# Performance work log

Hardware: AMD Instinct MI355X
Metric: run time of the kernel (lower is better)

## Reference

```python
import jax, jax.numpy as jnp
import numpy as np


def setup_inputs() -> dict:
    key = jax.random.key(0)
    k1, k2 = jax.random.split(key)
    queries = jax.random.normal(k1, (16, 1024, 256), dtype=jnp.float32)
    embedding = jax.random.normal(k2, (8192, 256), dtype=jnp.float32) * 0.02
    return {"queries": queries, "embedding": embedding}


def reference(queries, embedding):
    commitment_weight = 0.25
    # squared L2 distances: ||q||^2 + ||e||^2 - 2 q.e  -> [b, k, n]
    q_sq = jnp.sum(queries * queries, axis=-1, keepdims=True)          # [b,k,1]
    e_sq = jnp.sum(embedding * embedding, axis=-1)[None, None, :]      # [1,1,n]
    distances = q_sq + e_sq - 2.0 * jnp.einsum('bkc,nc->bkn', queries, embedding)
    code_indices = jnp.argmin(distances, axis=-1)                      # [b,k] int
    quantized = embedding[code_indices]                                # [b,k,c]
    commit_loss = jnp.mean((jax.lax.stop_gradient(queries) - quantized) ** 2)
    codebook_loss = jnp.mean((queries - jax.lax.stop_gradient(quantized)) ** 2)
    vq_loss = codebook_loss + commitment_weight * commit_loss
    # straight-through estimator
    quantized_st = queries + jax.lax.stop_gradient(quantized - queries)
    return (code_indices, quantized_st, vq_loss)
```

## Files before the change

### kernel.cpp

```cpp
#include <hip/hip_runtime.h>
#include <float.h>

typedef _Float16 half8 __attribute__((ext_vector_type(8)));
typedef _Float16 half4v __attribute__((ext_vector_type(4)));
typedef float f32x4 __attribute__((ext_vector_type(4)));

#define M_TOTAL 16384
#define N_CODES 8192
#define KDIM    256
#define BM 128
#define BN 256
#define BK 32
#define NK (KDIM / BK)
#define NB (N_CODES / BN)
#define TS 32
#define MARGIN 3.6e-3f
#define SQ_SCALE 512.0f
#define SE_SCALE 2048.0f
#define INV_PROD 1.9073486328125e-06f
#define RG 4
#define RCODES 1024
#define RNCH (N_CODES / RCODES)
#define RPB 1024
#define RM_BLOCKS 256
#define LR_BLOCKS 32

#define PREP_Q_BLOCKS (M_TOTAL / 4)
#define PREP_E_BLOCKS (N_CODES / 4)
#define TR_BLOCKS ((N_CODES / 64) * (KDIM / 64))

__device__ __forceinline__ void prep_body(const float* __restrict__ src,
                                          _Float16* __restrict__ dst,
                                          float* __restrict__ sq, float scale,
                                          int row0, int tid) {
    {
        const int r = row0 + (tid >> 6);
        const int e4 = tid & 63;
        const float4 v = *(const float4*)(src + (size_t)r * KDIM + e4 * 4);
        const half4v h = {(_Float16)(v.x * scale), (_Float16)(v.y * scale),
                          (_Float16)(v.z * scale), (_Float16)(v.w * scale)};
        ((half4v*)(dst + (size_t)r * KDIM))[e4] = h;
    }
    if (tid < 64) {
        const int grp = tid >> 4;
        const int sub = tid & 15;
        const int row = row0 + grp;
        const float* p = src + (size_t)row * KDIM + (sub >> 3) * 128 + (sub & 7);
        float r;
        {
            #pragma clang fp contract(off)
            float v = p[0];
            r = v * v;
            #pragma unroll
            for (int k = 1; k < 16; k++) { const float w = p[k * 8]; r = r + w * w; }
        }
        const float t1 = r  + __shfl_xor(r,  1, 64);
        const float t2 = t1 + __shfl_xor(t1, 2, 64);
        const float t3 = t2 + __shfl_xor(t2, 4, 64);
        const float t4 = t3 + __shfl_xor(t3, 8, 64);
        if (sub == 0) sq[row] = t4;
    }
}

__global__ void prep_fused_kernel(const float* __restrict__ Q, const float* __restrict__ E,
                                  _Float16* __restrict__ Qh, _Float16* __restrict__ Eh,
                                  float* __restrict__ qsq, float* __restrict__ esq,
                                  float* __restrict__ ET) {
    __shared__ float tile[64][65];
    const int tid = threadIdx.x;
    const int b = blockIdx.x;
    if (b < PREP_Q_BLOCKS) {
        prep_body(Q, Qh, qsq, SQ_SCALE, b * 4, tid);
        return;
    }
    if (b < PREP_Q_BLOCKS + PREP_E_BLOCKS) {
        prep_body(E, Eh, esq, SE_SCALE, (b - PREP_Q_BLOCKS) * 4, tid);
        return;
    }
    const int idx = b - PREP_Q_BLOCKS - PREP_E_BLOCKS;
    const int n0 = (idx & 127) * 64;
    const int k0 = (idx >> 7) * 64;
    const int r = tid >> 4;
    const int c4 = tid & 15;
    #pragma unroll
    for (int p = 0; p < 4; p++) {
        const int row = p * 16 + r;
        const float4 v = *(const float4*)(E + (size_t)(n0 + row) * KDIM + k0 + c4 * 4);
        tile[row][c4 * 4 + 0] = v.x;
        tile[row][c4 * 4 + 1] = v.y;
        tile[row][c4 * 4 + 2] = v.z;
        tile[row][c4 * 4 + 3] = v.w;
    }
    __syncthreads();
    #pragma unroll
    for (int p = 0; p < 4; p++) {
        const int d = p * 16 + r;
        float4 o;
        o.x = tile[c4 * 4 + 0][d];
        o.y = tile[c4 * 4 + 1][d];
        o.z = tile[c4 * 4 + 2][d];
        o.w = tile[c4 * 4 + 3][d];
        *(float4*)(ET + (size_t)(k0 + d) * N_CODES + n0 + c4 * 4) = o;
    }
}

union SMemU {
    struct { _Float16 q[3][BM * TS]; _Float16 e[3][BN * TS]; } t;
    struct { unsigned k1[BM][2]; unsigned k2[BM][2]; } red;
};

__device__ __forceinline__ void gl_lds16(const void* g, void* lds) {
    __builtin_amdgcn_global_load_lds(
        (const __attribute__((address_space(1))) unsigned*)g,
        (__attribute__((address_space(3))) unsigned*)lds, 16, 0, 0);
}

__global__ __launch_bounds__(256, 2)
void mfma_top2_kernel(const _Float16* __restrict__ Qh, const _Float16* __restrict__ Eh,
                      const float* __restrict__ esq,
                      unsigned* __restrict__ k1s, unsigned* __restrict__ k2s) {
    __shared__ SMemU sm;
    const int tid = threadIdx.x;
    const int m0 = blockIdx.x * BM;
    const int n0 = blockIdx.y * BN;
    const int w = tid >> 6, lane = tid & 63;
    const int wm = w >> 1, wn = w & 1;
    const int qd = lane >> 4, c = lane & 15;

    const int lrow = lane >> 2;
    const int gsw = (lane & 3) ^ ((lane >> 3) & 3);
    const _Float16* qsrc = Qh + (size_t)(m0 + w * 32 + lrow) * KDIM + gsw * 8;
    const _Float16* esrc = Eh + (size_t)(n0 + w * 64 + lrow) * KDIM + gsw * 8;

    f32x4 acc[4][8];
    const f32x4 zero = {0.f, 0.f, 0.f, 0.f};
    #pragma unroll
    for (int mt = 0; mt < 4; mt++)
        #pragma unroll
        for (int nt = 0; nt < 8; nt++) acc[mt][nt] = zero;

    #define STAGE(buf, kofs) do {                                                  \
        _Float16* qdst = sm.t.q[buf] + w * 1024;                                   \
        _Float16* edst = sm.t.e[buf] + w * 2048;                                   \
        gl_lds16(qsrc + (kofs),             qdst);                                 \
        gl_lds16(qsrc + 16 * KDIM + (kofs), qdst + 512);                           \
        gl_lds16(esrc + (kofs),             edst);                                 \
        gl_lds16(esrc + 16 * KDIM + (kofs), edst + 512);                           \
        gl_lds16(esrc + 32 * KDIM + (kofs), edst + 1024);                          \
        gl_lds16(esrc + 48 * KDIM + (kofs), edst + 1536);                          \
    } while (0)

    STAGE(0, 0);
    STAGE(1, BK);
    STAGE(2, 2 * BK);
    asm volatile("s_waitcnt vmcnt(12)" ::: "memory");
    __builtin_amdgcn_s_barrier();

    const int csw = (c >> 1) & 3;

    #pragma unroll
    for (int ki = 0; ki < NK; ki++) {
        const int buf = ki % 3;
        const _Float16* bq = sm.t.q[buf];
        const _Float16* be = sm.t.e[buf];
        half8 qa[4];
        #pragma unroll
        for (int mt = 0; mt < 4; mt++)
            qa[mt] = *(const half8*)(bq + (wm * 64 + mt * 16 + c) * TS + (qd ^ csw) * 8);
        __builtin_amdgcn_s_setprio(1);
        #pragma unroll
        for (int nt = 0; nt < 8; nt++) {
            const half8 eh = *(const half8*)(be + (wn * 128 + nt * 16 + c) * TS + (qd ^ csw) * 8);
            #pragma unroll
            for (int mt = 0; mt < 4; mt++)
                acc[mt][nt] = __builtin_amdgcn_mfma_f32_16x16x32_f16(qa[mt], eh, acc[mt][nt], 0, 0, 0);
        }
        __builtin_amdgcn_s_setprio(0);
        if (ki == NK - 1) break;
        if (ki <= NK - 3) { asm volatile("s_waitcnt vmcnt(6)" ::: "memory"); }
        else              { asm volatile("s_waitcnt vmcnt(0)" ::: "memory"); }
        __builtin_amdgcn_s_barrier();
        if (ki + 3 < NK) STAGE(buf, (ki + 3) * BK);
    }
    #undef STAGE

    float es8[8];
    #pragma unroll
    for (int nt = 0; nt < 8; nt++) es8[nt] = esq[n0 + wn * 128 + nt * 16 + c] + 8.0f;

    unsigned k1[16], k2[16];
    #pragma unroll
    for (int i = 0; i < 16; i++) { k1[i] = 0xFFFFFFFFu; k2[i] = 0xFFFFFFFFu; }

    #pragma unroll
    for (int mt = 0; mt < 4; mt++)
        #pragma unroll
        for (int nt = 0; nt < 8; nt++) {
            const unsigned nl = (unsigned)(wn * 128 + nt * 16 + c);
            #pragma unroll
            for (int r = 0; r < 4; r++) {
                const int i = mt * 4 + r;
                const float d = fmaf(acc[mt][nt][r], -INV_PROD, es8[nt]);
                const unsigned k = (__float_as_uint(d) & 0xFFFFFF00u) | nl;
                const unsigned t = min(k1[i], k);
                k2[i] = min(k2[i], max(k1[i], k));
                k1[i] = t;
            }
        }
    #pragma unroll
    for (int s = 1; s < 16; s <<= 1) {
        #pragma unroll
        for (int i = 0; i < 16; i++) {
            const unsigned ok1 = (unsigned)__shfl_xor((int)k1[i], s, 64);
            const unsigned ok2 = (unsigned)__shfl_xor((int)k2[i], s, 64);
            const unsigned t = min(k1[i], ok1);
            k2[i] = min(min(k2[i], ok2), max(k1[i], ok1));
            k1[i] = t;
        }
    }
    __syncthreads();
    if (c == 0) {
        #pragma unroll
        for (int mt = 0; mt < 4; mt++)
            #pragma unroll
            for (int r = 0; r < 4; r++) {
                const int ml = wm * 64 + mt * 16 + qd * 4 + r;
                sm.red.k1[ml][wn] = k1[mt * 4 + r];
                sm.red.k2[ml][wn] = k2[mt * 4 + r];
            }
    }
    __syncthreads();
    if (tid < BM) {
        const unsigned a1 = sm.red.k1[tid][0], b1 = sm.red.k1[tid][1];
        const unsigned a2 = sm.red.k2[tid][0], b2 = sm.red.k2[tid][1];
        const size_t o = (size_t)(m0 + tid) * NB + blockIdx.y;
        k1s[o] = min(a1, b1);
        k2s[o] = min(min(a2, b2), max(a1, b1));
    }
}

__global__ void finalize_kernel(const float* __restrict__ Q, const float* __restrict__ E,
                                const unsigned* __restrict__ k1s, const unsigned* __restrict__ k2s,
                                int* __restrict__ fcount, int* __restrict__ flist,
                                float* __restrict__ ws_loss, float* __restrict__ out) {
    const int q = blockIdx.x * 4 + (threadIdx.x >> 6);
    const int lane = threadIdx.x & 63;
    unsigned d1 = 0xFFFFFF00u;
    unsigned d2 = 0xFFFFFF00u;
    int gi = 0x7FFFFFFF;
    if (lane < NB) {
        const unsigned k1 = k1s[(size_t)q * NB + lane];
        const unsigned k2 = k2s[(size_t)q * NB + lane];
        d1 = k1 & 0xFFFFFF00u;
        gi = lane * BN + (int)(k1 & 255u);
        d2 = k2 & 0xFFFFFF00u;
    }
    #pragma unroll
    for (int s = 1; s < 64; s <<= 1) {
        const unsigned od1 = (unsigned)__shfl_xor((int)d1, s, 64);
        const int      ogi = __shfl_xor(gi, s, 64);
        const unsigned od2 = (unsigned)__shfl_xor((int)d2, s, 64);
        const unsigned nd2 = min(min(d2, od2), max(d1, od1));
        const bool take = (od1 < d1) || (od1 == d1 && ogi < gi);
        d1 = take ? od1 : d1;
        gi = take ? ogi : gi;
        d2 = nd2;
    }
    if ((__uint_as_float(d2) - __uint_as_float(d1)) < MARGIN) {
        if (lane == 0) flist[atomicAdd(fcount, 1)] = q;
        return;
    }

    if (lane == 0) out[q] = (float)gi;
    const float4 qv = *(const float4*)(Q + (size_t)q * KDIM + lane * 4);
    const float4 ev = *(const float4*)(E + (size_t)gi * KDIM + lane * 4);
    float4 st;
    {
        #pragma clang fp contract(off)
        st.x = qv.x + (ev.x - qv.x);
        st.y = qv.y + (ev.y - qv.y);
        st.z = qv.z + (ev.z - qv.z);
        st.w = qv.w + (ev.w - qv.w);
    }
    *(float4*)(out + M_TOTAL + (size_t)q * KDIM + lane * 4) = st;

    const float dx = qv.x - ev.x, dy = qv.y - ev.y, dz = qv.z - ev.z, dw = qv.w - ev.w;
    float s = dx * dx + dy * dy + dz * dz + dw * dw;
    #pragma unroll
    for (int off = 32; off > 0; off >>= 1) s += __shfl_down(s, off);
    if (lane == 0) ws_loss[q] = s;
}

__global__ __launch_bounds__(256, 4)
void refine_partial_kernel(const float* __restrict__ Q, const float* __restrict__ ET,
                           const float* __restrict__ qsq, const float* __restrict__ esq,
                           const int* __restrict__ fcount, const int* __restrict__ flist,
                           float* __restrict__ rp_v, int* __restrict__ rp_i) {
    const int cnt = *fcount;
    if (cnt == 0) return;
    const int ngroups = (cnt + RG - 1) / RG;
    const int ntasks = ngroups * RNCH;
    const int tid = threadIdx.x;
    const int w = tid >> 6, lane = tid & 63;
    __shared__ float qs[RG][KDIM];
    __shared__ float redv[4][RG];
    __shared__ int   redi[4][RG];

    for (int t = blockIdx.x; t < ntasks; t += RPB) {
        const int grp = t >> 3;
        const int chunk = t & (RNCH - 1);
        __syncthreads();
        {
            const int g = tid >> 6, c4 = tid & 63;
            const int fi = min(grp * RG + g, cnt - 1);
            const int q = flist[fi];
            *(float4*)&qs[g][c4 * 4] = *(const float4*)(Q + (size_t)q * KDIM + c4 * 4);
        }
        __syncthreads();

        const int nb = chunk * RCODES + tid * 4;
        float a[RG][4];
        #pragma unroll
        for (int g = 0; g < RG; g++)
            #pragma unroll
            for (int j = 0; j < 4; j++) a[g][j] = 0.f;

        for (int k4 = 0; k4 < KDIM / 4; k4++) {
            float4 qv[RG];
            #pragma unroll
            for (int g = 0; g < RG; g++) qv[g] = *(const float4*)&qs[g][k4 * 4];
            #pragma unroll
            for (int kk = 0; kk < 4; kk++) {
                const float4 ev = *(const float4*)(ET + (size_t)(k4 * 4 + kk) * N_CODES + nb);
                #pragma unroll
                for (int g = 0; g < RG; g++) {
                    const float qk = (kk == 0) ? qv[g].x : (kk == 1) ? qv[g].y
                                   : (kk == 2) ? qv[g].z : qv[g].w;
                    a[g][0] = fmaf(qk, ev.x, a[g][0]);
                    a[g][1] = fmaf(qk, ev.y, a[g][1]);
                    a[g][2] = fmaf(qk, ev.z, a[g][2]);
                    a[g][3] = fmaf(qk, ev.w, a[g][3]);
                }
            }
        }

        float es[4];
        #pragma unroll
        for (int j = 0; j < 4; j++) es[j] = esq[nb + j];

        #pragma unroll
        for (int g = 0; g < RG; g++) {
            const int fi = min(grp * RG + g, cnt - 1);
            const float qsv = qsq[flist[fi]];
            float bv = FLT_MAX; int bi = 0x7fffffff;
            #pragma unroll
            for (int j = 0; j < 4; j++) {
                float d;
                {
                    #pragma clang fp contract(off)
                    const float t1 = qsv + es[j];
                    d = t1 - 2.0f * a[g][j];
                }
                if (d < bv) { bv = d; bi = nb + j; }
            }
            #pragma unroll
            for (int s = 1; s < 64; s <<= 1) {
                const float ov = __shfl_xor(bv, s, 64);
                const int   oi = __shfl_xor(bi, s, 64);
                if (ov < bv || (ov == bv && oi < bi)) { bv = ov; bi = oi; }
            }
            if (lane == 0) { redv[w][g] = bv; redi[w][g] = bi; }
        }
        __syncthreads();
        if (tid < RG) {
            float fv = redv[0][tid]; int fidx = redi[0][tid];
            #pragma unroll
            for (int u = 1; u < 4; u++) {
                if (redv[u][tid] < fv || (redv[u][tid] == fv && redi[u][tid] < fidx)) {
                    fv = redv[u][tid]; fidx = redi[u][tid];
                }
            }
            rp_v[(size_t)t * RG + tid] = fv;
            rp_i[(size_t)t * RG + tid] = fidx;
        }
    }
}

__global__ void refine_merge_kernel(const float* __restrict__ Q, const float* __restrict__ E,
                                    const int* __restrict__ fcount, const int* __restrict__ flist,
                                    const float* __restrict__ rp_v, const int* __restrict__ rp_i,
                                    float* __restrict__ ws_loss, float* __restrict__ out) {
    const int cnt = *fcount;
    const int lane = threadIdx.x;
    for (int fi = blockIdx.x; fi < cnt; fi += RM_BLOCKS) {
        const int q = flist[fi];
        const int grp = fi >> 2, g = fi & 3;
        float bv = FLT_MAX; int bi = 0x7fffffff;
        if (lane < RNCH) {
            const size_t t = (size_t)(grp * RNCH + lane);
            bv = rp_v[t * RG + g];
            bi = rp_i[t * RG + g];
        }
        #pragma unroll
        for (int s = 1; s < 64; s <<= 1) {
            const float ov = __shfl_xor(bv, s, 64);
            const int   oi = __shfl_xor(bi, s, 64);
            if (ov < bv || (ov == bv && oi < bi)) { bv = ov; bi = oi; }
        }
        if (lane == 0) out[q] = (float)bi;

        const float4 qv = *(const float4*)(Q + (size_t)q * KDIM + lane * 4);
        const float4 ev = *(const float4*)(E + (size_t)bi * KDIM + lane * 4);
        float4 st;
        {
            #pragma clang fp contract(off)
            st.x = qv.x + (ev.x - qv.x);
            st.y = qv.y + (ev.y - qv.y);
            st.z = qv.z + (ev.z - qv.z);
            st.w = qv.w + (ev.w - qv.w);
        }
        *(float4*)(out + M_TOTAL + (size_t)q * KDIM + lane * 4) = st;
        const float dx = qv.x - ev.x, dy = qv.y - ev.y, dz = qv.z - ev.z, dw = qv.w - ev.w;
        float s = dx * dx + dy * dy + dz * dz + dw * dw;
        #pragma unroll
        for (int off = 32; off > 0; off >>= 1) s += __shfl_down(s, off);
        if (lane == 0) ws_loss[q] = s;
    }
}

__global__ void loss_reduce_kernel(const float* __restrict__ ws_loss, float* __restrict__ out) {
    const int tid = threadIdx.x;
    float s = 0.f;
    for (int i = blockIdx.x * 256 + tid; i < M_TOTAL; i += LR_BLOCKS * 256)
        s += ws_loss[i];
    #pragma unroll
    for (int off = 32; off > 0; off >>= 1) s += __shfl_down(s, off);
    __shared__ float ws[4];
    if ((tid & 63) == 0) ws[tid >> 6] = s;
    __syncthreads();
    if (tid == 0) {
        const float tot = (ws[0] + ws[1]) + (ws[2] + ws[3]);
        atomicAdd(out + M_TOTAL + (size_t)M_TOTAL * KDIM,
                  tot * (1.25f / (float)((size_t)M_TOTAL * KDIM)));
    }
}

extern "C" void kernel_launch(void* const* d_in, const int* in_sizes, int n_in,
                              void* d_out, int out_size, void* d_ws, size_t ws_size,
                              hipStream_t stream) {
    const float* Q = (const float*)d_in[0];
    const float* E = (const float*)d_in[1];
    float* out = (float*)d_out;

    char* ws = (char*)d_ws;
    _Float16* Qh  = (_Float16*)(ws);
    _Float16* Eh  = (_Float16*)(ws + (size_t)8  * 1024 * 1024);
    float* qsq    = (float*)   (ws + (size_t)12 * 1024 * 1024);
    float* esq    = qsq + M_TOTAL;
    unsigned* k1s = (unsigned*)(ws + (size_t)13 * 1024 * 1024);
    unsigned* k2s = (unsigned*)(ws + (size_t)17 * 1024 * 1024);
    int*   fcount = (int*)     (ws + (size_t)25 * 1024 * 1024);
    int*   flist  = fcount + 64;
    float* ws_loss= (float*)   (ws + (size_t)25 * 1024 * 1024 + 512 * 1024);
    float* ET     = (float*)   (ws + (size_t)26 * 1024 * 1024);
    float* rp_v   = (float*)k1s;
    int*   rp_i   = (int*)k2s;

    hipMemsetAsync(out + M_TOTAL + (size_t)M_TOTAL * KDIM, 0, sizeof(float), stream);
    hipMemsetAsync(fcount, 0, sizeof(int), stream);

    prep_fused_kernel<<<PREP_Q_BLOCKS + PREP_E_BLOCKS + TR_BLOCKS, 256, 0, stream>>>(
        Q, E, Qh, Eh, qsq, esq, ET);

    mfma_top2_kernel<<<dim3(M_TOTAL / BM, N_CODES / BN), 256, 0, stream>>>(
        Qh, Eh, esq, k1s, k2s);

    finalize_kernel<<<M_TOTAL / 4, 256, 0, stream>>>(Q, E, k1s, k2s, fcount, flist, ws_loss, out);
    refine_partial_kernel<<<RPB, 256, 0, stream>>>(Q, ET, qsq, esq, fcount, flist, rp_v, rp_i);
    refine_merge_kernel<<<RM_BLOCKS, 64, 0, stream>>>(Q, E, fcount, flist, rp_v, rp_i, ws_loss, out);
    loss_reduce_kernel<<<LR_BLOCKS, 256, 0, stream>>>(ws_loss, out);
}
```

Baseline: 216.9 us.

## Refine only candidate code blocks per flagged query and fuse refine stages

The fp32 refinement of ambiguous queries now scans only the 256-code blocks whose per-block best fp16 distance lies within a margin of the global best, using per-block minima from the top-2 pass, instead of all 8192 codes. The partial and merge refine kernels are fused into one kernel with one block per flagged query, which removes a launch and the intermediate buffers. The two memsets are folded into the prep kernel to cut launch overhead. Correctness now depends on the per-block keys bounding the true minimum within MARGIN. Each query is processed alone, so ET rows are no longer shared across four queries.

```diff
diff --git a/kernel.cpp b/kernel.cpp
--- a/kernel.cpp
+++ b/kernel.cpp
@@ -18,11 +18,7 @@
 #define SQ_SCALE 512.0f
 #define SE_SCALE 2048.0f
 #define INV_PROD 1.9073486328125e-06f
-#define RG 4
-#define RCODES 1024
-#define RNCH (N_CODES / RCODES)
-#define RPB 1024
-#define RM_BLOCKS 256
+#define RB 1024
 #define LR_BLOCKS 32
 
 #define PREP_Q_BLOCKS (M_TOTAL / 4)
@@ -65,10 +61,12 @@
 __global__ void prep_fused_kernel(const float* __restrict__ Q, const float* __restrict__ E,
                                   _Float16* __restrict__ Qh, _Float16* __restrict__ Eh,
                                   float* __restrict__ qsq, float* __restrict__ esq,
-                                  float* __restrict__ ET) {
+                                  float* __restrict__ ET,
+                                  int* __restrict__ fcount, float* __restrict__ loss_slot) {
     __shared__ float tile[64][65];
     const int tid = threadIdx.x;
     const int b = blockIdx.x;
+    if (b == 0 && tid == 0) { *fcount = 0; *loss_slot = 0.f; }
     if (b < PREP_Q_BLOCKS) {
         prep_body(Q, Qh, qsq, SQ_SCALE, b * 4, tid);
         return;
@@ -292,114 +290,57 @@
 }
 
 __global__ __launch_bounds__(256, 4)
-void refine_partial_kernel(const float* __restrict__ Q, const float* __restrict__ ET,
-                           const float* __restrict__ qsq, const float* __restrict__ esq,
-                           const int* __restrict__ fcount, const int* __restrict__ flist,
-                           float* __restrict__ rp_v, int* __restrict__ rp_i) {
+void refine_kernel(const float* __restrict__ Q, const float* __restrict__ E,
+                   const float* __restrict__ ET,
+                   const float* __restrict__ qsq, const float* __restrict__ esq,
+                   const int* __restrict__ fcount, const int* __restrict__ flist,
+                   const unsigned* __restrict__ k1s,
+                   float* __restrict__ ws_loss, float* __restrict__ out) {
     const int cnt = *fcount;
-    if (cnt == 0) return;
-    const int ngroups = (cnt + RG - 1) / RG;
-    const int ntasks = ngroups * RNCH;
     const int tid = threadIdx.x;
     const int w = tid >> 6, lane = tid & 63;
-    __shared__ float qs[RG][KDIM];
-    __shared__ float redv[4][RG];
-    __shared__ int   redi[4][RG];
-
-    for (int t = blockIdx.x; t < ntasks; t += RPB) {
-        const int grp = t >> 3;
-        const int chunk = t & (RNCH - 1);
+    __shared__ float qs[KDIM];
+    __shared__ unsigned cmask_sh;
+    __shared__ float redv[4];
+    __shared__ int   redi[4];
+
+    for (int fi = blockIdx.x; fi < cnt; fi += RB) {
+        const int q = flist[fi];
         __syncthreads();
-        {
-            const int g = tid >> 6, c4 = tid & 63;
-            const int fi = min(grp * RG + g, cnt - 1);
-            const int q = flist[fi];
-            *(float4*)&qs[g][c4 * 4] = *(const float4*)(Q + (size_t)q * KDIM + c4 * 4);
+        qs[tid] = Q[(size_t)q * KDIM + tid];
+        if (w == 0) {
+            unsigned k1 = 0xFFFFFF00u;
+            if (lane < NB) k1 = k1s[(size_t)q * NB + lane];
+            unsigned m = k1;
+            #pragma unroll
+            for (int s = 1; s < 64; s <<= 1)
+                m = min(m, (unsigned)__shfl_xor((int)m, s, 64));
+            const float thr = __uint_as_float(m & 0xFFFFFF00u) + MARGIN;
+            const bool cand = (lane < NB) &&
+                              (__uint_as_float(k1 & 0xFFFFFF00u) < thr);
+            const unsigned long long bal = __ballot(cand);
+            if (lane == 0) cmask_sh = (unsigned)bal;
         }
         __syncthreads();
-
-        const int nb = chunk * RCODES + tid * 4;
-        float a[RG][4];
-        #pragma unroll
-        for (int g = 0; g < RG; g++)
-            #pragma unroll
-            for (int j = 0; j < 4; j++) a[g][j] = 0.f;
-
-        for (int k4 = 0; k4 < KDIM / 4; k4++) {
-            float4 qv[RG];
-            #pragma unroll
-            for (int g = 0; g < RG; g++) qv[g] = *(const float4*)&qs[g][k4 * 4];
-            #pragma unroll
-            for (int kk = 0; kk < 4; kk++) {
-                const float4 ev = *(const float4*)(ET + (size_t)(k4 * 4 + kk) * N_CODES + nb);
-                #pragma unroll
-                for (int g = 0; g < RG; g++) {
-                    const float qk = (kk == 0) ? qv[g].x : (kk == 1) ? qv[g].y
-                                   : (kk == 2) ? qv[g].z : qv[g].w;
-                    a[g][0] = fmaf(qk, ev.x, a[g][0]);
-                    a[g][1] = fmaf(qk, ev.y, a[g][1]);
-                    a[g][2] = fmaf(qk, ev.z, a[g][2]);
-                    a[g][3] = fmaf(qk, ev.w, a[g][3]);
-                }
+        unsigned cmask = cmask_sh;
+        const float qsv = qsq[q];
+        float bv = FLT_MAX;
+        int   bi = 0x7fffffff;
+        while (cmask) {
+            const int cb = __builtin_ctz(cmask);
+            cmask &= cmask - 1;
+            const int n = cb * BN + tid;
+            float a = 0.f;
+            #pragma unroll 8
+            for (int k = 0; k < KDIM; k++)
+                a = fmaf(qs[k], ET[(size_t)k * N_CODES + n], a);
+            float d;
+            {
+                #pragma clang fp contract(off)
+                const float t1 = qsv + esq[n];
+                d = t1 - 2.0f * a;
             }
-        }
-
-        float es[4];
-        #pragma unroll
-        for (int j = 0; j < 4; j++) es[j] = esq[nb + j];
-
-        #pragma unroll
-        for (int g = 0; g < RG; g++) {
-            const int fi = min(grp * RG + g, cnt - 1);
-            const float qsv = qsq[flist[fi]];
-            float bv = FLT_MAX; int bi = 0x7fffffff;
-            #pragma unroll
-            for (int j = 0; j < 4; j++) {
-                float d;
-                {
-                    #pragma clang fp contract(off)
-                    const float t1 = qsv + es[j];
-                    d = t1 - 2.0f * a[g][j];
-                }
-                if (d < bv) { bv = d; bi = nb + j; }
-            }
-            #pragma unroll
-            for (int s = 1; s < 64; s <<= 1) {
-                const float ov = __shfl_xor(bv, s, 64);
-                const int   oi = __shfl_xor(bi, s, 64);
-                if (ov < bv || (ov == bv && oi < bi)) { bv = ov; bi = oi; }
-            }
-            if (lane == 0) { redv[w][g] = bv; redi[w][g] = bi; }
-        }
-        __syncthreads();
-        if (tid < RG) {
-            float fv = redv[0][tid]; int fidx = redi[0][tid];
-            #pragma unroll
-            for (int u = 1; u < 4; u++) {
-                if (redv[u][tid] < fv || (redv[u][tid] == fv && redi[u][tid] < fidx)) {
-                    fv = redv[u][tid]; fidx = redi[u][tid];
-                }
-            }
-            rp_v[(size_t)t * RG + tid] = fv;
-            rp_i[(size_t)t * RG + tid] = fidx;
-        }
-    }
-}
-
-__global__ void refine_merge_kernel(const float* __restrict__ Q, const float* __restrict__ E,
-                                    const int* __restrict__ fcount, const int* __restrict__ flist,
-                                    const float* __restrict__ rp_v, const int* __restrict__ rp_i,
-                                    float* __restrict__ ws_loss, float* __restrict__ out) {
-    const int cnt = *fcount;
-    const int lane = threadIdx.x;
-    for (int fi = blockIdx.x; fi < cnt; fi += RM_BLOCKS) {
-        const int q = flist[fi];
-        const int grp = fi >> 2, g = fi & 3;
-        float bv = FLT_MAX; int bi = 0x7fffffff;
-        if (lane < RNCH) {
-            const size_t t = (size_t)(grp * RNCH + lane);
-            bv = rp_v[t * RG + g];
-            bi = rp_i[t * RG + g];
+            if (d < bv || (d == bv && n < bi)) { bv = d; bi = n; }
         }
         #pragma unroll
         for (int s = 1; s < 64; s <<= 1) {
@@ -407,24 +348,35 @@
             const int   oi = __shfl_xor(bi, s, 64);
             if (ov < bv || (ov == bv && oi < bi)) { bv = ov; bi = oi; }
         }
-        if (lane == 0) out[q] = (float)bi;
-
-        const float4 qv = *(const float4*)(Q + (size_t)q * KDIM + lane * 4);
-        const float4 ev = *(const float4*)(E + (size_t)bi * KDIM + lane * 4);
-        float4 st;
-        {
-            #pragma clang fp contract(off)
-            st.x = qv.x + (ev.x - qv.x);
-            st.y = qv.y + (ev.y - qv.y);
-            st.z = qv.z + (ev.z - qv.z);
-            st.w = qv.w + (ev.w - qv.w);
-        }
-        *(float4*)(out + M_TOTAL + (size_t)q * KDIM + lane * 4) = st;
-        const float dx = qv.x - ev.x, dy = qv.y - ev.y, dz = qv.z - ev.z, dw = qv.w - ev.w;
-        float s = dx * dx + dy * dy + dz * dz + dw * dw;
-        #pragma unroll
-        for (int off = 32; off > 0; off >>= 1) s += __shfl_down(s, off);
-        if (lane == 0) ws_loss[q] = s;
+        if (lane == 0) { redv[w] = bv; redi[w] = bi; }
+        __syncthreads();
+        float fv = redv[0]; int fidx = redi[0];
+        #pragma unroll
+        for (int u = 1; u < 4; u++) {
+            if (redv[u] < fv || (redv[u] == fv && redi[u] < fidx)) {
+                fv = redv[u]; fidx = redi[u];
+            }
+        }
+        if (w == 0) {
+            if (lane == 0) out[q] = (float)fidx;
+            const float4 qv = *(const float4*)(Q + (size_t)q * KDIM + lane * 4);
+            const float4 ev = *(const float4*)(E + (size_t)fidx * KDIM + lane * 4);
+            float4 st;
+            {
+                #pragma clang fp contract(off)
+                st.x = qv.x + (ev.x - qv.x);
+                st.y = qv.y + (ev.y - qv.y);
+                st.z = qv.z + (ev.z - qv.z);
+                st.w = qv.w + (ev.w - qv.w);
+            }
+            *(float4*)(out + M_TOTAL + (size_t)q * KDIM + lane * 4) = st;
+            const float dx = qv.x - ev.x, dy = qv.y - ev.y;
+            const float dz = qv.z - ev.z, dw = qv.w - ev.w;
+            float s = dx * dx + dy * dy + dz * dz + dw * dw;
+            #pragma unroll
+            for (int off = 32; off > 0; off >>= 1) s += __shfl_down(s, off);
+            if (lane == 0) ws_loss[q] = s;
+        }
     }
 }
 
@@ -463,20 +415,15 @@
     int*   flist  = fcount + 64;
     float* ws_loss= (float*)   (ws + (size_t)25 * 1024 * 1024 + 512 * 1024);
     float* ET     = (float*)   (ws + (size_t)26 * 1024 * 1024);
-    float* rp_v   = (float*)k1s;
-    int*   rp_i   = (int*)k2s;
-
-    hipMemsetAsync(out + M_TOTAL + (size_t)M_TOTAL * KDIM, 0, sizeof(float), stream);
-    hipMemsetAsync(fcount, 0, sizeof(int), stream);
+    float* loss_slot = out + M_TOTAL + (size_t)M_TOTAL * KDIM;
 
     prep_fused_kernel<<<PREP_Q_BLOCKS + PREP_E_BLOCKS + TR_BLOCKS, 256, 0, stream>>>(
-        Q, E, Qh, Eh, qsq, esq, ET);
+        Q, E, Qh, Eh, qsq, esq, ET, fcount, loss_slot);
 
     mfma_top2_kernel<<<dim3(M_TOTAL / BM, N_CODES / BN), 256, 0, stream>>>(
         Qh, Eh, esq, k1s, k2s);
 
     finalize_kernel<<<M_TOTAL / 4, 256, 0, stream>>>(Q, E, k1s, k2s, fcount, flist, ws_loss, out);
-    refine_partial_kernel<<<RPB, 256, 0, stream>>>(Q, ET, qsq, esq, fcount, flist, rp_v, rp_i);
-    refine_merge_kernel<<<RM_BLOCKS, 64, 0, stream>>>(Q, E, fcount, flist, rp_v, rp_i, ws_loss, out);
+    refine_kernel<<<RB, 256, 0, stream>>>(Q, E, ET, qsq, esq, fcount, flist, k1s, ws_loss, out);
     loss_reduce_kernel<<<LR_BLOCKS, 256, 0, stream>>>(ws_loss, out);
 }
```

New measurement: 216.3 us. About the same (-0.3%).
